# Kernel optimization log

Hardware: AMD Instinct MI355X
Metric: run time of the kernel (lower is better)

## Reference

```python
import jax, jax.numpy as jnp
import numpy as np

NUM_HEADS = 16
D_MODEL = 1024
D_KV = 64
NUM_BUCKETS = 32
MAX_DISTANCE = 128


def _relative_position_bucket(relative_position, num_buckets=NUM_BUCKETS, max_distance=MAX_DISTANCE):
    # faithful port of the torch static method (bidirectional variant)
    n = -relative_position
    nb = num_buckets // 2
    ret = (n < 0).astype(jnp.int32) * nb
    n = jnp.abs(n)
    max_exact = nb // 2
    is_small = n < max_exact
    # guard log(0); is_small branch covers n < max_exact anyway
    val_if_large = max_exact + (
        jnp.log(jnp.maximum(n, 1).astype(jnp.float32) / max_exact)
        / np.log(max_distance / max_exact)
        * (nb - max_exact)
    ).astype(jnp.int32)
    val_if_large = jnp.minimum(val_if_large, nb - 1)
    return ret + jnp.where(is_small, n, val_if_large)


def _compute_bias(seq_len, rel_bias):
    ctx = jnp.arange(seq_len)[:, None]
    mem = jnp.arange(seq_len)[None, :]
    bucket = _relative_position_bucket(mem - ctx)  # [S, S]
    values = rel_bias[bucket]                      # [S, S, H]
    return jnp.transpose(values, (2, 0, 1))[None]  # [1, H, S, S]


def setup_inputs() -> dict:
    key = jax.random.key(0)
    ks = jax.random.split(key, 6)
    B, S = 4, 1024
    scale = 1.0 / np.sqrt(D_MODEL)
    return {
        "hidden_states": jax.random.normal(ks[0], (B, S, D_MODEL), jnp.float32),
        "attention_mask": jnp.ones((B, 1, 1, S), jnp.int32),
        "Wq": jax.random.normal(ks[1], (NUM_HEADS * D_KV, D_MODEL), jnp.float32) * scale,
        "Wk": jax.random.normal(ks[2], (NUM_HEADS * D_KV, D_MODEL), jnp.float32) * scale,
        "Wv": jax.random.normal(ks[3], (NUM_HEADS * D_KV, D_MODEL), jnp.float32) * scale,
        "Wo": jax.random.normal(ks[4], (D_MODEL, NUM_HEADS * D_KV), jnp.float32) * scale,
        "rel_bias": jax.random.normal(ks[5], (NUM_BUCKETS, NUM_HEADS), jnp.float32),
    }


def reference(hidden_states, attention_mask, Wq, Wk, Wv, Wo, rel_bias):
    B, S, _ = hidden_states.shape
    # projections (Linear with bias=False: x @ W.T), reshape to [B, S, H, d_kv]
    q = jnp.einsum('bsd,ed->bse', hidden_states, Wq).reshape(B, S, NUM_HEADS, D_KV)
    k = jnp.einsum('bsd,ed->bse', hidden_states, Wk).reshape(B, S, NUM_HEADS, D_KV)
    v = jnp.einsum('bsd,ed->bse', hidden_states, Wv).reshape(B, S, NUM_HEADS, D_KV)
    scores = jnp.einsum('bqhd,bkhd->bhqk', q, k) / np.sqrt(D_KV)
    scores = scores + _compute_bias(S, rel_bias)
    scores = jnp.where(attention_mask == 0, jnp.float32(-1e9), scores)
    attn_weights = jax.nn.softmax(scores, axis=-1)  # dropout is identity at eval
    attn_output = jnp.einsum('bhqk,bkhd->bqhd', attn_weights, v).reshape(B, S, NUM_HEADS * D_KV)
    output = jnp.einsum('bse,de->bsd', attn_output, Wo)
    return output, attn_weights
```

## Files before the change

### kernel.cpp

```cpp
#include <hip/hip_runtime.h>
#include <hip/hip_bf16.h>

#define BB 4
#define SS 1024
#define HH 16
#define DK 64
#define DM 1024
#define MM (BB * SS)

typedef __attribute__((ext_vector_type(8))) short bh8_t;
typedef __attribute__((ext_vector_type(4))) float f4_t;

#define MFMA(a, b, c) __builtin_amdgcn_mfma_f32_16x16x32_bf16(a, b, c, 0, 0, 0)

__device__ __forceinline__ short f2bf(float f) {
    unsigned u = __builtin_bit_cast(unsigned, f);
    u = (u + 0x7FFFu + ((u >> 16) & 1u)) >> 16;
    return (short)u;
}
__device__ __forceinline__ float bf2f(short h) {
    unsigned u = ((unsigned)(unsigned short)h) << 16;
    return __builtin_bit_cast(float, u);
}

__device__ __forceinline__ int rel_bucket(int rel) {
    int n = -rel;
    int ret = 0;
    if (n < 0) { ret = 16; n = -n; }
    int v;
    if (n < 8) {
        v = n;
    } else {
        float t = logf((float)n * 0.125f) / 2.7725887298583984f * 8.0f;
        v = 8 + (int)t;
        if (v > 15) v = 15;
    }
    return ret + v;
}

__global__ __launch_bounds__(256)
void k_split(const float* __restrict__ X, const float* __restrict__ Wq,
             const float* __restrict__ Wk, const float* __restrict__ Wv,
             const float* __restrict__ Wo, const float* __restrict__ rbv,
             short* __restrict__ Xh, short* __restrict__ Xl,
             short* __restrict__ Wqh, short* __restrict__ Wql,
             short* __restrict__ Wkh, short* __restrict__ Wkl,
             short* __restrict__ Wvh, short* __restrict__ Woh,
             float* __restrict__ biasT) {
    const long i = (long)blockIdx.x * 256 + threadIdx.x;
    if (i < 2097152) {
        const float* src;
        short* dh;
        short* dl = nullptr;
        long j = i;
        if (i < 1048576) { src = X; dh = Xh; dl = Xl; }
        else if (i < 1310720) { src = Wq; dh = Wqh; dl = Wql; j = i - 1048576; }
        else if (i < 1572864) { src = Wk; dh = Wkh; dl = Wkl; j = i - 1310720; }
        else if (i < 1835008) { src = Wv; dh = Wvh; j = i - 1572864; }
        else { src = Wo; dh = Woh; j = i - 1835008; }
        f4_t v = *(const f4_t*)(src + j * 4);
        short4 h, l;
        h.x = f2bf(v[0]); l.x = f2bf(v[0] - bf2f(h.x));
        h.y = f2bf(v[1]); l.y = f2bf(v[1] - bf2f(h.y));
        h.z = f2bf(v[2]); l.z = f2bf(v[2] - bf2f(h.z));
        h.w = f2bf(v[3]); l.w = f2bf(v[3] - bf2f(h.w));
        *(short4*)(dh + j * 4) = h;
        if (dl) *(short4*)(dl + j * 4) = l;
    } else if (i < 2105408) {
        const long j = i - 2097152;
        const int hd = (int)(j / 516);
        const int d0 = (int)(j % 516) * 4;
#pragma unroll
        for (int t = 0; t < 4; ++t) {
            const int dd = d0 + t;
            biasT[hd * 2064 + dd] = rbv[rel_bucket(dd - 1024) * HH + hd];
        }
    }
}

__global__ __launch_bounds__(256)
void k_proj(const short* __restrict__ Xh, const short* __restrict__ Xl,
            const short* __restrict__ Wqh, const short* __restrict__ Wql,
            const short* __restrict__ Wkh, const short* __restrict__ Wkl,
            const short* __restrict__ Wvh,
            short* __restrict__ Qh, short* __restrict__ Ql,
            short* __restrict__ Kh, short* __restrict__ Kl,
            short* __restrict__ Vt) {
    const int z = blockIdx.z;

    __shared__ short Ah[128][40], Al[128][40], Bh[128][40], Bl[128][40];

    const int tid = threadIdx.x;
    const int m0 = blockIdx.y * 128, n0 = blockIdx.x * 128;
    const int wave = tid >> 6, lane = tid & 63;
    const int quad = lane >> 4, lm = lane & 15;
    const int wm = (wave >> 1) * 64, wn = (wave & 1) * 64;
    const int r = tid >> 1, sg = (tid & 1) * 16;

    f4_t acc[4][4];
#pragma unroll
    for (int i = 0; i < 4; ++i)
#pragma unroll
        for (int j = 0; j < 4; ++j) acc[i][j] = (f4_t){0.f, 0.f, 0.f, 0.f};

    const size_t xoff = (size_t)(m0 + r) * DM + sg;
    const size_t woff = (size_t)(n0 + r) * DM + sg;

    if (z < 2) {
        const short* Wh = z ? Wkh : Wqh;
        const short* Wl = z ? Wkl : Wql;
        short* Oh = z ? Kh : Qh;
        short* Ol = z ? Kl : Ql;

        uint4 a0 = *(const uint4*)(Xh + xoff), a1 = *(const uint4*)(Xh + xoff + 8);
        uint4 c0 = *(const uint4*)(Xl + xoff), c1 = *(const uint4*)(Xl + xoff + 8);
        uint4 b0 = *(const uint4*)(Wh + woff), b1 = *(const uint4*)(Wh + woff + 8);
        uint4 d0 = *(const uint4*)(Wl + woff), d1 = *(const uint4*)(Wl + woff + 8);

        for (int k0 = 0; k0 < DM; k0 += 32) {
            __syncthreads();
            *(uint4*)&Ah[r][sg] = a0; *(uint4*)&Ah[r][sg + 8] = a1;
            *(uint4*)&Al[r][sg] = c0; *(uint4*)&Al[r][sg + 8] = c1;
            *(uint4*)&Bh[r][sg] = b0; *(uint4*)&Bh[r][sg + 8] = b1;
            *(uint4*)&Bl[r][sg] = d0; *(uint4*)&Bl[r][sg + 8] = d1;
            __syncthreads();
            if (k0 + 32 < DM) {
                const size_t xo = xoff + k0 + 32, wo = woff + k0 + 32;
                a0 = *(const uint4*)(Xh + xo); a1 = *(const uint4*)(Xh + xo + 8);
                c0 = *(const uint4*)(Xl + xo); c1 = *(const uint4*)(Xl + xo + 8);
                b0 = *(const uint4*)(Wh + wo); b1 = *(const uint4*)(Wh + wo + 8);
                d0 = *(const uint4*)(Wl + wo); d1 = *(const uint4*)(Wl + wo + 8);
            }

            bh8_t ah[4], al[4];
#pragma unroll
            for (int i = 0; i < 4; ++i) {
                ah[i] = *(const bh8_t*)&Ah[wm + i * 16 + lm][quad * 8];
                al[i] = *(const bh8_t*)&Al[wm + i * 16 + lm][quad * 8];
            }
#pragma unroll
            for (int j = 0; j < 4; ++j) {
                bh8_t bhj = *(const bh8_t*)&Bh[wn + j * 16 + lm][quad * 8];
                bh8_t blj = *(const bh8_t*)&Bl[wn + j * 16 + lm][quad * 8];
#pragma unroll
                for (int i = 0; i < 4; ++i) {
                    acc[i][j] = MFMA(al[i], bhj, acc[i][j]);
                    acc[i][j] = MFMA(ah[i], blj, acc[i][j]);
                    acc[i][j] = MFMA(ah[i], bhj, acc[i][j]);
                }
            }
        }

#pragma unroll
        for (int i = 0; i < 4; ++i)
#pragma unroll
            for (int j = 0; j < 4; ++j)
#pragma unroll
                for (int g = 0; g < 4; ++g) {
                    const int row = m0 + wm + i * 16 + quad * 4 + g;
                    const int col = n0 + wn + j * 16 + lm;
                    const int b = row >> 10, s = row & 1023;
                    const int hd = col >> 6, dk = col & 63;
                    const float v = acc[i][j][g];
                    const short vh = f2bf(v);
                    const short vl = f2bf(v - bf2f(vh));
                    const size_t o = ((size_t)((b * HH + hd) * SS + s)) * DK + dk;
                    Oh[o] = vh;
                    Ol[o] = vl;
                }
    } else {
        uint4 a0 = *(const uint4*)(Xh + xoff), a1 = *(const uint4*)(Xh + xoff + 8);
        uint4 b0 = *(const uint4*)(Wvh + woff), b1 = *(const uint4*)(Wvh + woff + 8);

        for (int k0 = 0; k0 < DM; k0 += 32) {
            __syncthreads();
            *(uint4*)&Ah[r][sg] = a0; *(uint4*)&Ah[r][sg + 8] = a1;
            *(uint4*)&Bh[r][sg] = b0; *(uint4*)&Bh[r][sg + 8] = b1;
            __syncthreads();
            if (k0 + 32 < DM) {
                const size_t xo = xoff + k0 + 32, wo = woff + k0 + 32;
                a0 = *(const uint4*)(Xh + xo); a1 = *(const uint4*)(Xh + xo + 8);
                b0 = *(const uint4*)(Wvh + wo); b1 = *(const uint4*)(Wvh + wo + 8);
            }

            bh8_t ah[4];
#pragma unroll
            for (int i = 0; i < 4; ++i)
                ah[i] = *(const bh8_t*)&Ah[wm + i * 16 + lm][quad * 8];
#pragma unroll
            for (int j = 0; j < 4; ++j) {
                bh8_t bhj = *(const bh8_t*)&Bh[wn + j * 16 + lm][quad * 8];
#pragma unroll
                for (int i = 0; i < 4; ++i) acc[i][j] = MFMA(ah[i], bhj, acc[i][j]);
            }
        }

#pragma unroll
        for (int i = 0; i < 4; ++i)
#pragma unroll
            for (int j = 0; j < 4; ++j)
#pragma unroll
                for (int g = 0; g < 4; ++g) {
                    const int row = m0 + wm + i * 16 + quad * 4 + g;
                    const int col = n0 + wn + j * 16 + lm;
                    const int b = row >> 10, s = row & 1023;
                    const int hd = col >> 6, dk = col & 63;
                    Vt[((size_t)((b * HH + hd) * DK + dk)) * SS + s] = f2bf(acc[i][j][g]);
                }
    }
}

#define EPAD 1044

__global__ __launch_bounds__(512, 4)
void k_fused(const short* __restrict__ Qh, const short* __restrict__ Ql,
             const short* __restrict__ Kh, const short* __restrict__ Kl,
             const short* __restrict__ Vt, const int* __restrict__ mask,
             const float* __restrict__ biasT, float* __restrict__ P,
             short* __restrict__ AO) {
    __shared__ __align__(16) char smem[75584];
    float* E     = (float*)smem;
    float* redS  = (float*)smem;
    float* biasS = (float*)(smem + 66816);
    int*   maskS = (int*)(smem + 70976);
    float* wmaxS = (float*)(smem + 75072);

    const int tid = threadIdx.x;
    const int bid = blockIdx.x;
    const int swz = (bid & 7) * 512 + (bid >> 3);
    const int qb = swz & 63, bh = swz >> 6;
    const int b = bh >> 4, hd = bh & 15;
    const int q0 = qb * 16;
    const int wave = tid >> 6, lane = tid & 63;
    const int quad = lane >> 4, lm = lane & 15;

    for (int i = tid; i < 1040; i += 512)
        biasS[i] = biasT[hd * 2064 + i + 1009 - q0];
    for (int i = tid; i < 1024; i += 512) maskS[i] = mask[b * SS + i];

    bh8_t qah[2], qal[2];
#pragma unroll
    for (int ks = 0; ks < 2; ++ks) {
        const size_t qo = ((size_t)bh * SS + q0 + lm) * DK + ks * 32 + quad * 8;
        qah[ks] = *(const bh8_t*)(Qh + qo);
        qal[ks] = *(const bh8_t*)(Ql + qo);
    }
    __syncthreads();

    float pmax[4] = {-3.0e38f, -3.0e38f, -3.0e38f, -3.0e38f};

    bh8_t kh[2][2][2], kl[2][2][2];
    {
        const int kb = wave * 128;
#pragma unroll
        for (int j = 0; j < 2; ++j)
#pragma unroll
            for (int ks = 0; ks < 2; ++ks) {
                const size_t ko =
                    ((size_t)bh * SS + kb + j * 16 + lm) * DK + ks * 32 + quad * 8;
                kh[0][j][ks] = *(const bh8_t*)(Kh + ko);
                kl[0][j][ks] = *(const bh8_t*)(Kl + ko);
            }
    }
#pragma unroll
    for (int kt = 0; kt < 4; ++kt) {
        const int cur = kt & 1;
        if (kt < 3) {
            const int kb2 = wave * 128 + (kt + 1) * 32;
#pragma unroll
            for (int j = 0; j < 2; ++j)
#pragma unroll
                for (int ks = 0; ks < 2; ++ks) {
                    const size_t ko =
                        ((size_t)bh * SS + kb2 + j * 16 + lm) * DK + ks * 32 + quad * 8;
                    kh[cur ^ 1][j][ks] = *(const bh8_t*)(Kh + ko);
                    kl[cur ^ 1][j][ks] = *(const bh8_t*)(Kl + ko);
                }
        }
        const int kb = wave * 128 + kt * 32;
        f4_t acc[2];
        acc[0] = (f4_t){0.f, 0.f, 0.f, 0.f};
        acc[1] = (f4_t){0.f, 0.f, 0.f, 0.f};
#pragma unroll
        for (int j = 0; j < 2; ++j)
#pragma unroll
            for (int ks = 0; ks < 2; ++ks) {
                acc[j] = MFMA(qal[ks], kh[cur][j][ks], acc[j]);
                acc[j] = MFMA(qah[ks], kl[cur][j][ks], acc[j]);
                acc[j] = MFMA(qah[ks], kh[cur][j][ks], acc[j]);
            }
#pragma unroll
        for (int j = 0; j < 2; ++j) {
            const int col = kb + j * 16 + lm;
            const int msk = maskS[col];
#pragma unroll
            for (int g = 0; g < 4; ++g) {
                const int rl = quad * 4 + g;
                float s = acc[j][g] * 0.125f + biasS[col - rl + 15];
                s = (msk == 0) ? -1e9f : s;
                E[rl * EPAD + col] = s;
                pmax[g] = fmaxf(pmax[g], s);
            }
        }
    }
#pragma unroll
    for (int g = 0; g < 4; ++g) {
        float m = pmax[g];
        m = fmaxf(m, __shfl_xor(m, 1, 64));
        m = fmaxf(m, __shfl_xor(m, 2, 64));
        m = fmaxf(m, __shfl_xor(m, 4, 64));
        m = fmaxf(m, __shfl_xor(m, 8, 64));
        if (lm == 0) wmaxS[wave * 16 + quad * 4 + g] = m;
    }
    __syncthreads();

    {
        const int row = tid >> 5;
        const int cc = (tid & 31) * 4;
        float m = wmaxS[row];
#pragma unroll
        for (int w = 1; w < 8; ++w) m = fmaxf(m, wmaxS[w * 16 + row]);
        f4_t ev[8];
        float sum = 0.f;
#pragma unroll
        for (int u = 0; u < 8; ++u) {
            f4_t s4 = *(const f4_t*)&E[row * EPAD + cc + u * 128];
            f4_t e;
            e[0] = __expf(s4[0] - m);
            e[1] = __expf(s4[1] - m);
            e[2] = __expf(s4[2] - m);
            e[3] = __expf(s4[3] - m);
            ev[u] = e;
            sum += e[0] + e[1] + e[2] + e[3];
        }
        sum += __shfl_xor(sum, 1, 64);
        sum += __shfl_xor(sum, 2, 64);
        sum += __shfl_xor(sum, 4, 64);
        sum += __shfl_xor(sum, 8, 64);
        sum += __shfl_xor(sum, 16, 64);
        const float inv = 1.0f / sum;
#pragma unroll
        for (int u = 0; u < 8; ++u) {
            f4_t p;
            p[0] = ev[u][0] * inv;
            p[1] = ev[u][1] * inv;
            p[2] = ev[u][2] * inv;
            p[3] = ev[u][3] * inv;
            *(f4_t*)&E[row * EPAD + cc + u * 128] = p;
        }
    }
    __syncthreads();

    f4_t acc[4];
#pragma unroll
    for (int f = 0; f < 4; ++f) acc[f] = (f4_t){0.f, 0.f, 0.f, 0.f};

    bh8_t vb[2][4];
    {
        const int kg0 = wave * 128 + quad * 8;
#pragma unroll
        for (int f = 0; f < 4; ++f)
            vb[0][f] = *(const bh8_t*)(Vt + ((size_t)bh * DK + f * 16 + lm) * SS + kg0);
    }
#pragma unroll
    for (int kk = 0; kk < 4; ++kk) {
        const int cur = kk & 1;
        const int kg = wave * 128 + kk * 32 + quad * 8;
        f4_t p0 = *(const f4_t*)&E[lm * EPAD + kg];
        f4_t p1 = *(const f4_t*)&E[lm * EPAD + kg + 4];
        if (kk < 3) {
            const int kg2 = wave * 128 + (kk + 1) * 32 + quad * 8;
#pragma unroll
            for (int f = 0; f < 4; ++f)
                vb[cur ^ 1][f] =
                    *(const bh8_t*)(Vt + ((size_t)bh * DK + f * 16 + lm) * SS + kg2);
        }
        bh8_t pa;
        pa[0] = f2bf(p0[0]); pa[1] = f2bf(p0[1]);
        pa[2] = f2bf(p0[2]); pa[3] = f2bf(p0[3]);
        pa[4] = f2bf(p1[0]); pa[5] = f2bf(p1[1]);
        pa[6] = f2bf(p1[2]); pa[7] = f2bf(p1[3]);
#pragma unroll
        for (int f = 0; f < 4; ++f) acc[f] = MFMA(pa, vb[cur][f], acc[f]);
    }

    {
        const int c0 = (lane & 31) * 4;
        const int rh = lane >> 5;
#pragma unroll
        for (int u = 0; u < 8; ++u) {
            const int rr = u * 2 + rh;
            f4_t pv = *(const f4_t*)&E[rr * EPAD + wave * 128 + c0];
            __builtin_nontemporal_store(
                pv, (f4_t*)(P + ((size_t)bh * SS + q0 + rr) * SS + wave * 128 + c0));
        }
    }

    asm volatile("s_waitcnt lgkmcnt(0)" ::: "memory");
    __builtin_amdgcn_sched_barrier(0);
    __builtin_amdgcn_s_barrier();
    __builtin_amdgcn_sched_barrier(0);

#pragma unroll
    for (int f = 0; f < 4; ++f)
#pragma unroll
        for (int g = 0; g < 4; ++g)
            redS[((size_t)wave * 16 + quad * 4 + g) * 64 + f * 16 + lm] = acc[f][g];

    asm volatile("s_waitcnt lgkmcnt(0)" ::: "memory");
    __builtin_amdgcn_sched_barrier(0);
    __builtin_amdgcn_s_barrier();
    __builtin_amdgcn_sched_barrier(0);

    {
        const int flat = tid * 2;
        const int q = flat >> 6, dk = flat & 63;
        float s0 = 0.f, s1 = 0.f;
#pragma unroll
        for (int w = 0; w < 8; ++w) {
            s0 += redS[((size_t)w * 16 + q) * 64 + dk];
            s1 += redS[((size_t)w * 16 + q) * 64 + dk + 1];
        }
        short2 o;
        o.x = f2bf(s0);
        o.y = f2bf(s1);
        *(short2*)(AO + ((size_t)(b * SS + q0 + q)) * DM + hd * DK + dk) = o;
    }
}

__global__ __launch_bounds__(256)
void k_out(const short* __restrict__ A, const short* __restrict__ Woh,
           float* __restrict__ Out) {
    __shared__ short As[128][40], Bs[128][40];

    const int tid = threadIdx.x;
    const int m0 = blockIdx.y * 128, n0 = blockIdx.x * 128;
    const int wave = tid >> 6, lane = tid & 63;
    const int quad = lane >> 4, lm = lane & 15;
    const int wm = (wave >> 1) * 64, wn = (wave & 1) * 64;
    const int r = tid >> 1, sg = (tid & 1) * 16;

    f4_t acc[4][4];
#pragma unroll
    for (int i = 0; i < 4; ++i)
#pragma unroll
        for (int j = 0; j < 4; ++j) acc[i][j] = (f4_t){0.f, 0.f, 0.f, 0.f};

    const size_t aoff = (size_t)(m0 + r) * DM + sg;
    const size_t woff = (size_t)(n0 + r) * DM + sg;
    uint4 a0 = *(const uint4*)(A + aoff), a1 = *(const uint4*)(A + aoff + 8);
    uint4 b0 = *(const uint4*)(Woh + woff), b1 = *(const uint4*)(Woh + woff + 8);

    for (int k0 = 0; k0 < DM; k0 += 32) {
        __syncthreads();
        *(uint4*)&As[r][sg] = a0; *(uint4*)&As[r][sg + 8] = a1;
        *(uint4*)&Bs[r][sg] = b0; *(uint4*)&Bs[r][sg + 8] = b1;
        __syncthreads();
        if (k0 + 32 < DM) {
            const size_t ao = aoff + k0 + 32, wo = woff + k0 + 32;
            a0 = *(const uint4*)(A + ao); a1 = *(const uint4*)(A + ao + 8);
            b0 = *(const uint4*)(Woh + wo); b1 = *(const uint4*)(Woh + wo + 8);
        }

        bh8_t ah[4];
#pragma unroll
        for (int i = 0; i < 4; ++i)
            ah[i] = *(const bh8_t*)&As[wm + i * 16 + lm][quad * 8];
#pragma unroll
        for (int j = 0; j < 4; ++j) {
            bh8_t bhj = *(const bh8_t*)&Bs[wn + j * 16 + lm][quad * 8];
#pragma unroll
            for (int i = 0; i < 4; ++i) acc[i][j] = MFMA(ah[i], bhj, acc[i][j]);
        }
    }

#pragma unroll
    for (int i = 0; i < 4; ++i)
#pragma unroll
        for (int j = 0; j < 4; ++j)
#pragma unroll
            for (int g = 0; g < 4; ++g)
                __builtin_nontemporal_store(
                    acc[i][j][g],
                    &Out[(size_t)(m0 + wm + i * 16 + quad * 4 + g) * DM + n0 + wn +
                         j * 16 + lm]);
}

extern "C" void kernel_launch(void* const* d_in, const int* in_sizes, int n_in,
                              void* d_out, int out_size, void* d_ws, size_t ws_size,
                              hipStream_t stream) {
    const float* X    = (const float*)d_in[0];
    const int*   mask = (const int*)d_in[1];
    const float* Wq   = (const float*)d_in[2];
    const float* Wk   = (const float*)d_in[3];
    const float* Wv   = (const float*)d_in[4];
    const float* Wo   = (const float*)d_in[5];
    const float* rb   = (const float*)d_in[6];

    float* out = (float*)d_out;
    float* P   = out + (size_t)BB * SS * DM;

    short* ws = (short*)d_ws;
    short* Qh  = ws;
    short* Ql  = ws + (size_t)4194304;
    short* Kh  = ws + (size_t)8388608;
    short* Kl  = ws + (size_t)12582912;
    short* Vt  = ws + (size_t)16777216;
    short* AO  = ws + (size_t)20971520;
    short* Xh  = ws + (size_t)25165824;
    short* Xl  = ws + (size_t)29360128;
    short* Wqh = ws + (size_t)33554432;
    short* Wql = ws + (size_t)34603008;
    short* Wkh = ws + (size_t)35651584;
    short* Wkl = ws + (size_t)36700160;
    short* Wvh = ws + (size_t)37748736;
    short* Woh = ws + (size_t)38797312;
    float* biasT = (float*)((char*)d_ws + 79691776);

    k_split<<<dim3(8225), 256, 0, stream>>>(X, Wq, Wk, Wv, Wo, rb, Xh, Xl, Wqh,
                                            Wql, Wkh, Wkl, Wvh, Woh, biasT);
    k_proj <<<dim3(8, 32, 3), 256, 0, stream>>>(Xh, Xl, Wqh, Wql, Wkh, Wkl, Wvh,
                                                Qh, Ql, Kh, Kl, Vt);
    k_fused<<<dim3(4096), 512, 0, stream>>>(Qh, Ql, Kh, Kl, Vt, mask, biasT, P, AO);
    k_out  <<<dim3(8, 32), 256, 0, stream>>>(AO, Woh, out);
}
```

Measured before the change: 566.5 us.

## Use direct global-to-LDS loads in GEMMs and drop max pass in softmax

The projection and output GEMMs now use global_load_lds to copy tiles straight into unpadded shared memory instead of staging through registers. This removes register prefetch but also loses the overlap of the next tile's load with compute, and the unpadded layout may cause LDS bank conflicts. The fused attention kernel skips the row-max pass, exponentiates scores directly while summing, and normalises once when writing P and the PV result, reading bias and mask from global instead of LDS. Without max subtraction the softmax can overflow if scores grow large.

```diff
diff --git a/kernel.cpp b/kernel.cpp
--- a/kernel.cpp
+++ b/kernel.cpp
@@ -21,6 +21,12 @@
 __device__ __forceinline__ float bf2f(short h) {
     unsigned u = ((unsigned)(unsigned short)h) << 16;
     return __builtin_bit_cast(float, u);
+}
+
+__device__ __forceinline__ void gl16(const short* g, short* l) {
+    __builtin_amdgcn_global_load_lds(
+        (const __attribute__((address_space(1))) void*)g,
+        (__attribute__((address_space(3))) void*)l, 16, 0, 0);
 }
 
 __device__ __forceinline__ int rel_bucket(int rel) {
@@ -88,23 +94,22 @@
             short* __restrict__ Vt) {
     const int z = blockIdx.z;
 
-    __shared__ short Ah[128][40], Al[128][40], Bh[128][40], Bl[128][40];
+    __shared__ short AhL[4096], AlL[4096], BhL[4096], BlL[4096];
 
     const int tid = threadIdx.x;
     const int m0 = blockIdx.y * 128, n0 = blockIdx.x * 128;
     const int wave = tid >> 6, lane = tid & 63;
     const int quad = lane >> 4, lm = lane & 15;
     const int wm = (wave >> 1) * 64, wn = (wave & 1) * 64;
-    const int r = tid >> 1, sg = (tid & 1) * 16;
+
+    const int sr = wave * 32 + (lane >> 2);
+    const int sc = (lane & 3) * 8;
 
     f4_t acc[4][4];
 #pragma unroll
     for (int i = 0; i < 4; ++i)
 #pragma unroll
         for (int j = 0; j < 4; ++j) acc[i][j] = (f4_t){0.f, 0.f, 0.f, 0.f};
-
-    const size_t xoff = (size_t)(m0 + r) * DM + sg;
-    const size_t woff = (size_t)(n0 + r) * DM + sg;
 
     if (z < 2) {
         const short* Wh = z ? Wkh : Wqh;
@@ -112,36 +117,29 @@
         short* Oh = z ? Kh : Qh;
         short* Ol = z ? Kl : Ql;
 
-        uint4 a0 = *(const uint4*)(Xh + xoff), a1 = *(const uint4*)(Xh + xoff + 8);
-        uint4 c0 = *(const uint4*)(Xl + xoff), c1 = *(const uint4*)(Xl + xoff + 8);
-        uint4 b0 = *(const uint4*)(Wh + woff), b1 = *(const uint4*)(Wh + woff + 8);
-        uint4 d0 = *(const uint4*)(Wl + woff), d1 = *(const uint4*)(Wl + woff + 8);
-
         for (int k0 = 0; k0 < DM; k0 += 32) {
+            if (k0) __syncthreads();
+#pragma unroll
+            for (int j = 0; j < 2; ++j) {
+                const int row = sr + j * 16;
+                const int le = row * 32 + sc;
+                gl16(Xh + (size_t)(m0 + row) * DM + k0 + sc, &AhL[le]);
+                gl16(Xl + (size_t)(m0 + row) * DM + k0 + sc, &AlL[le]);
+                gl16(Wh + (size_t)(n0 + row) * DM + k0 + sc, &BhL[le]);
+                gl16(Wl + (size_t)(n0 + row) * DM + k0 + sc, &BlL[le]);
+            }
             __syncthreads();
-            *(uint4*)&Ah[r][sg] = a0; *(uint4*)&Ah[r][sg + 8] = a1;
-            *(uint4*)&Al[r][sg] = c0; *(uint4*)&Al[r][sg + 8] = c1;
-            *(uint4*)&Bh[r][sg] = b0; *(uint4*)&Bh[r][sg + 8] = b1;
-            *(uint4*)&Bl[r][sg] = d0; *(uint4*)&Bl[r][sg + 8] = d1;
-            __syncthreads();
-            if (k0 + 32 < DM) {
-                const size_t xo = xoff + k0 + 32, wo = woff + k0 + 32;
-                a0 = *(const uint4*)(Xh + xo); a1 = *(const uint4*)(Xh + xo + 8);
-                c0 = *(const uint4*)(Xl + xo); c1 = *(const uint4*)(Xl + xo + 8);
-                b0 = *(const uint4*)(Wh + wo); b1 = *(const uint4*)(Wh + wo + 8);
-                d0 = *(const uint4*)(Wl + wo); d1 = *(const uint4*)(Wl + wo + 8);
-            }
 
             bh8_t ah[4], al[4];
 #pragma unroll
             for (int i = 0; i < 4; ++i) {
-                ah[i] = *(const bh8_t*)&Ah[wm + i * 16 + lm][quad * 8];
-                al[i] = *(const bh8_t*)&Al[wm + i * 16 + lm][quad * 8];
+                ah[i] = *(const bh8_t*)&AhL[(wm + i * 16 + lm) * 32 + quad * 8];
+                al[i] = *(const bh8_t*)&AlL[(wm + i * 16 + lm) * 32 + quad * 8];
             }
 #pragma unroll
             for (int j = 0; j < 4; ++j) {
-                bh8_t bhj = *(const bh8_t*)&Bh[wn + j * 16 + lm][quad * 8];
-                bh8_t blj = *(const bh8_t*)&Bl[wn + j * 16 + lm][quad * 8];
+                bh8_t bhj = *(const bh8_t*)&BhL[(wn + j * 16 + lm) * 32 + quad * 8];
+                bh8_t blj = *(const bh8_t*)&BlL[(wn + j * 16 + lm) * 32 + quad * 8];
 #pragma unroll
                 for (int i = 0; i < 4; ++i) {
                     acc[i][j] = MFMA(al[i], bhj, acc[i][j]);
@@ -169,27 +167,24 @@
                     Ol[o] = vl;
                 }
     } else {
-        uint4 a0 = *(const uint4*)(Xh + xoff), a1 = *(const uint4*)(Xh + xoff + 8);
-        uint4 b0 = *(const uint4*)(Wvh + woff), b1 = *(const uint4*)(Wvh + woff + 8);
-
         for (int k0 = 0; k0 < DM; k0 += 32) {
+            if (k0) __syncthreads();
+#pragma unroll
+            for (int j = 0; j < 2; ++j) {
+                const int row = sr + j * 16;
+                const int le = row * 32 + sc;
+                gl16(Xh + (size_t)(m0 + row) * DM + k0 + sc, &AhL[le]);
+                gl16(Wvh + (size_t)(n0 + row) * DM + k0 + sc, &BhL[le]);
+            }
             __syncthreads();
-            *(uint4*)&Ah[r][sg] = a0; *(uint4*)&Ah[r][sg + 8] = a1;
-            *(uint4*)&Bh[r][sg] = b0; *(uint4*)&Bh[r][sg + 8] = b1;
-            __syncthreads();
-            if (k0 + 32 < DM) {
-                const size_t xo = xoff + k0 + 32, wo = woff + k0 + 32;
-                a0 = *(const uint4*)(Xh + xo); a1 = *(const uint4*)(Xh + xo + 8);
-                b0 = *(const uint4*)(Wvh + wo); b1 = *(const uint4*)(Wvh + wo + 8);
-            }
 
             bh8_t ah[4];
 #pragma unroll
             for (int i = 0; i < 4; ++i)
-                ah[i] = *(const bh8_t*)&Ah[wm + i * 16 + lm][quad * 8];
+                ah[i] = *(const bh8_t*)&AhL[(wm + i * 16 + lm) * 32 + quad * 8];
 #pragma unroll
             for (int j = 0; j < 4; ++j) {
-                bh8_t bhj = *(const bh8_t*)&Bh[wn + j * 16 + lm][quad * 8];
+                bh8_t bhj = *(const bh8_t*)&BhL[(wn + j * 16 + lm) * 32 + quad * 8];
 #pragma unroll
                 for (int i = 0; i < 4; ++i) acc[i][j] = MFMA(ah[i], bhj, acc[i][j]);
             }
@@ -218,12 +213,10 @@
              const short* __restrict__ Vt, const int* __restrict__ mask,
              const float* __restrict__ biasT, float* __restrict__ P,
              short* __restrict__ AO) {
-    __shared__ __align__(16) char smem[75584];
+    __shared__ __align__(16) char smem[67328];
     float* E     = (float*)smem;
     float* redS  = (float*)smem;
-    float* biasS = (float*)(smem + 66816);
-    int*   maskS = (int*)(smem + 70976);
-    float* wmaxS = (float*)(smem + 75072);
+    float* wsumS = (float*)(smem + 66816);
 
     const int tid = threadIdx.x;
     const int bid = blockIdx.x;
@@ -234,9 +227,8 @@
     const int wave = tid >> 6, lane = tid & 63;
     const int quad = lane >> 4, lm = lane & 15;
 
-    for (int i = tid; i < 1040; i += 512)
-        biasS[i] = biasT[hd * 2064 + i + 1009 - q0];
-    for (int i = tid; i < 1024; i += 512) maskS[i] = mask[b * SS + i];
+    const float* biasRow = biasT + hd * 2064 + 1024 - q0;
+    const int* maskRow = mask + b * SS;
 
     bh8_t qah[2], qal[2];
 #pragma unroll
@@ -245,9 +237,8 @@
         qah[ks] = *(const bh8_t*)(Qh + qo);
         qal[ks] = *(const bh8_t*)(Ql + qo);
     }
-    __syncthreads();
-
-    float pmax[4] = {-3.0e38f, -3.0e38f, -3.0e38f, -3.0e38f};
+
+    float psum[4] = {0.f, 0.f, 0.f, 0.f};
 
     bh8_t kh[2][2][2], kl[2][2][2];
     {
@@ -292,68 +283,27 @@
 #pragma unroll
         for (int j = 0; j < 2; ++j) {
             const int col = kb + j * 16 + lm;
-            const int msk = maskS[col];
+            const int msk = maskRow[col];
 #pragma unroll
             for (int g = 0; g < 4; ++g) {
                 const int rl = quad * 4 + g;
-                float s = acc[j][g] * 0.125f + biasS[col - rl + 15];
+                float s = acc[j][g] * 0.125f + biasRow[col - rl];
                 s = (msk == 0) ? -1e9f : s;
-                E[rl * EPAD + col] = s;
-                pmax[g] = fmaxf(pmax[g], s);
+                const float e = __expf(s);
+                E[rl * EPAD + col] = e;
+                psum[g] += e;
             }
         }
     }
 #pragma unroll
     for (int g = 0; g < 4; ++g) {
-        float m = pmax[g];
-        m = fmaxf(m, __shfl_xor(m, 1, 64));
-        m = fmaxf(m, __shfl_xor(m, 2, 64));
-        m = fmaxf(m, __shfl_xor(m, 4, 64));
-        m = fmaxf(m, __shfl_xor(m, 8, 64));
-        if (lm == 0) wmaxS[wave * 16 + quad * 4 + g] = m;
-    }
-    __syncthreads();
-
-    {
-        const int row = tid >> 5;
-        const int cc = (tid & 31) * 4;
-        float m = wmaxS[row];
-#pragma unroll
-        for (int w = 1; w < 8; ++w) m = fmaxf(m, wmaxS[w * 16 + row]);
-        f4_t ev[8];
-        float sum = 0.f;
-#pragma unroll
-        for (int u = 0; u < 8; ++u) {
-            f4_t s4 = *(const f4_t*)&E[row * EPAD + cc + u * 128];
-            f4_t e;
-            e[0] = __expf(s4[0] - m);
-            e[1] = __expf(s4[1] - m);
-            e[2] = __expf(s4[2] - m);
-            e[3] = __expf(s4[3] - m);
-            ev[u] = e;
-            sum += e[0] + e[1] + e[2] + e[3];
-        }
-        sum += __shfl_xor(sum, 1, 64);
-        sum += __shfl_xor(sum, 2, 64);
-        sum += __shfl_xor(sum, 4, 64);
-        sum += __shfl_xor(sum, 8, 64);
-        sum += __shfl_xor(sum, 16, 64);
-        const float inv = 1.0f / sum;
-#pragma unroll
-        for (int u = 0; u < 8; ++u) {
-            f4_t p;
-            p[0] = ev[u][0] * inv;
-            p[1] = ev[u][1] * inv;
-            p[2] = ev[u][2] * inv;
-            p[3] = ev[u][3] * inv;
-            *(f4_t*)&E[row * EPAD + cc + u * 128] = p;
-        }
-    }
-    __syncthreads();
-
-    f4_t acc[4];
-#pragma unroll
-    for (int f = 0; f < 4; ++f) acc[f] = (f4_t){0.f, 0.f, 0.f, 0.f};
+        float p = psum[g];
+        p += __shfl_xor(p, 1, 64);
+        p += __shfl_xor(p, 2, 64);
+        p += __shfl_xor(p, 4, 64);
+        p += __shfl_xor(p, 8, 64);
+        if (lm == 0) wsumS[(quad * 4 + g) * 8 + wave] = p;
+    }
 
     bh8_t vb[2][4];
     {
@@ -362,6 +312,32 @@
         for (int f = 0; f < 4; ++f)
             vb[0][f] = *(const bh8_t*)(Vt + ((size_t)bh * DK + f * 16 + lm) * SS + kg0);
     }
+    __syncthreads();
+
+    auto invRow = [&](int r) -> float {
+        f4_t a = *(const f4_t*)&wsumS[r * 8];
+        f4_t c = *(const f4_t*)&wsumS[r * 8 + 4];
+        return 1.0f / (a[0] + a[1] + a[2] + a[3] + c[0] + c[1] + c[2] + c[3]);
+    };
+
+    {
+        const int c0 = (lane & 31) * 4;
+        const int rh = lane >> 5;
+#pragma unroll
+        for (int u = 0; u < 8; ++u) {
+            const int rr = u * 2 + rh;
+            const float iv = invRow(rr);
+            f4_t pv = *(const f4_t*)&E[rr * EPAD + wave * 128 + c0];
+            pv[0] *= iv; pv[1] *= iv; pv[2] *= iv; pv[3] *= iv;
+            __builtin_nontemporal_store(
+                pv, (f4_t*)(P + ((size_t)bh * SS + q0 + rr) * SS + wave * 128 + c0));
+        }
+    }
+
+    f4_t acc[4];
+#pragma unroll
+    for (int f = 0; f < 4; ++f) acc[f] = (f4_t){0.f, 0.f, 0.f, 0.f};
+
 #pragma unroll
     for (int kk = 0; kk < 4; ++kk) {
         const int cur = kk & 1;
@@ -384,17 +360,9 @@
         for (int f = 0; f < 4; ++f) acc[f] = MFMA(pa, vb[cur][f], acc[f]);
     }
 
-    {
-        const int c0 = (lane & 31) * 4;
-        const int rh = lane >> 5;
-#pragma unroll
-        for (int u = 0; u < 8; ++u) {
-            const int rr = u * 2 + rh;
-            f4_t pv = *(const f4_t*)&E[rr * EPAD + wave * 128 + c0];
-            __builtin_nontemporal_store(
-                pv, (f4_t*)(P + ((size_t)bh * SS + q0 + rr) * SS + wave * 128 + c0));
-        }
-    }
+    float ivg[4];
+#pragma unroll
+    for (int g = 0; g < 4; ++g) ivg[g] = invRow(quad * 4 + g);
 
     asm volatile("s_waitcnt lgkmcnt(0)" ::: "memory");
     __builtin_amdgcn_sched_barrier(0);
@@ -405,7 +373,8 @@
     for (int f = 0; f < 4; ++f)
 #pragma unroll
         for (int g = 0; g < 4; ++g)
-            redS[((size_t)wave * 16 + quad * 4 + g) * 64 + f * 16 + lm] = acc[f][g];
+            redS[((size_t)wave * 16 + quad * 4 + g) * 64 + f * 16 + lm] =
+                acc[f][g] * ivg[g];
 
     asm volatile("s_waitcnt lgkmcnt(0)" ::: "memory");
     __builtin_amdgcn_sched_barrier(0);
@@ -431,14 +400,16 @@
 __global__ __launch_bounds__(256)
 void k_out(const short* __restrict__ A, const short* __restrict__ Woh,
            float* __restrict__ Out) {
-    __shared__ short As[128][40], Bs[128][40];
+    __shared__ short AsL[4096], BsL[4096];
 
     const int tid = threadIdx.x;
     const int m0 = blockIdx.y * 128, n0 = blockIdx.x * 128;
     const int wave = tid >> 6, lane = tid & 63;
     const int quad = lane >> 4, lm = lane & 15;
     const int wm = (wave >> 1) * 64, wn = (wave & 1) * 64;
-    const int r = tid >> 1, sg = (tid & 1) * 16;
+
+    const int sr = wave * 32 + (lane >> 2);
+    const int sc = (lane & 3) * 8;
 
     f4_t acc[4][4];
 #pragma unroll
@@ -446,29 +417,24 @@
 #pragma unroll
         for (int j = 0; j < 4; ++j) acc[i][j] = (f4_t){0.f, 0.f, 0.f, 0.f};
 
-    const size_t aoff = (size_t)(m0 + r) * DM + sg;
-    const size_t woff = (size_t)(n0 + r) * DM + sg;
-    uint4 a0 = *(const uint4*)(A + aoff), a1 = *(const uint4*)(A + aoff + 8);
-    uint4 b0 = *(const uint4*)(Woh + woff), b1 = *(const uint4*)(Woh + woff + 8);
-
     for (int k0 = 0; k0 < DM; k0 += 32) {
+        if (k0) __syncthreads();
+#pragma unroll
+        for (int j = 0; j < 2; ++j) {
+            const int row = sr + j * 16;
+            const int le = row * 32 + sc;
+            gl16(A + (size_t)(m0 + row) * DM + k0 + sc, &AsL[le]);
+            gl16(Woh + (size_t)(n0 + row) * DM + k0 + sc, &BsL[le]);
+        }
         __syncthreads();
-        *(uint4*)&As[r][sg] = a0; *(uint4*)&As[r][sg + 8] = a1;
-        *(uint4*)&Bs[r][sg] = b0; *(uint4*)&Bs[r][sg + 8] = b1;
-        __syncthreads();
-        if (k0 + 32 < DM) {
-            const size_t ao = aoff + k0 + 32, wo = woff + k0 + 32;
-            a0 = *(const uint4*)(A + ao); a1 = *(const uint4*)(A + ao + 8);
-            b0 = *(const uint4*)(Woh + wo); b1 = *(const uint4*)(Woh + wo + 8);
-        }
 
         bh8_t ah[4];
 #pragma unroll
         for (int i = 0; i < 4; ++i)
-            ah[i] = *(const bh8_t*)&As[wm + i * 16 + lm][quad * 8];
+            ah[i] = *(const bh8_t*)&AsL[(wm + i * 16 + lm) * 32 + quad * 8];
 #pragma unroll
         for (int j = 0; j < 4; ++j) {
-            bh8_t bhj = *(const bh8_t*)&Bs[wn + j * 16 + lm][quad * 8];
+            bh8_t bhj = *(const bh8_t*)&BsL[(wn + j * 16 + lm) * 32 + quad * 8];
 #pragma unroll
             for (int i = 0; i < 4; ++i) acc[i][j] = MFMA(ah[i], bhj, acc[i][j]);
         }
```

Measured after the change: 554.5 us. 2.1% less time.
